# Kernel tuning notes

Hardware: AMD Instinct MI355X
Metric: run time of the kernel (lower is better)

The kernel has to match this reference:

```python
import jax, jax.numpy as jnp
import numpy as np

K = 20          # num neighbors (init kwarg k)
BN_EPS = 1e-5   # PyTorch BatchNorm default eps


def setup_inputs() -> dict:
    key = jax.random.key(0)
    k1, k2 = jax.random.split(key, 2)
    x = jax.random.normal(k1, (8, 64, 4096), dtype=jnp.float32)       # (b, d, n)
    w = jax.random.normal(k2, (64, 128), dtype=jnp.float32) * 0.05    # Conv2d 1x1: (out=64, in=2*64)
    gamma = jnp.ones((64,), jnp.float32)    # BatchNorm1d weight
    beta = jnp.zeros((64,), jnp.float32)    # BatchNorm1d bias
    return {"x": x, "w": w, "gamma": gamma, "beta": beta}


def reference(x, w, gamma, beta):
    # x: (b, d, n)
    xt = jnp.swapaxes(x, 1, 2)                       # (b, n, d)
    # kNN via pairwise squared euclidean distance (same ordering as torch.cdist)
    sq = jnp.sum(xt * xt, axis=-1)                   # (b, n)
    d2 = sq[:, :, None] + sq[:, None, :] - 2.0 * jnp.einsum('bnd,bmd->bnm', xt, xt)
    _, idx = jax.lax.top_k(-d2, K)                   # (b, n, K) smallest distances
    # gather neighbor features: (b, n, K, d)
    nb = jax.vmap(lambda pts, i: pts[i])(xt, idx)
    ctr = xt[:, :, None, :]                          # (b, n, 1, d)
    # edge feature = concat([neighbor - x, x]) -> (b, n, K, 2d)
    feat = jnp.concatenate([nb - ctr, jnp.broadcast_to(ctr, nb.shape)], axis=-1)
    # 1x1 conv (no bias) then max over neighbors
    h = jnp.max(jnp.einsum('bnkc,oc->bnko', feat, w), axis=2)   # (b, n, out)
    # BatchNorm1d (training mode: batch statistics over (b, n), biased var)
    mean = jnp.mean(h, axis=(0, 1))
    var = jnp.mean((h - mean) ** 2, axis=(0, 1))
    hn = (h - mean) / jnp.sqrt(var + BN_EPS) * gamma + beta
    out = jax.nn.gelu(hn, approximate=False)         # exact GELU (PyTorch default)
    return jnp.swapaxes(out, 1, 2)                   # (b, out, n)
```

## Files before the change

### kernel.cpp

```cpp
#include <hip/hip_runtime.h>

#define BIGF 3.402823466e38f

typedef __attribute__((ext_vector_type(8))) short bf16x8;
typedef __attribute__((ext_vector_type(4))) float f32x4;

__device__ __forceinline__ void gload_lds16(const float* g, float* lds) {
  __builtin_amdgcn_global_load_lds((const __attribute__((address_space(1))) void*)g,
                                   (__attribute__((address_space(3))) void*)lds, 16, 0, 0);
}
__device__ __forceinline__ void gload_lds16u(const unsigned short* g, unsigned short* lds) {
  __builtin_amdgcn_global_load_lds((const __attribute__((address_space(1))) void*)g,
                                   (__attribute__((address_space(3))) void*)lds, 16, 0, 0);
}

__device__ __forceinline__ unsigned short bf16_rne(float f) {
  unsigned int u = __float_as_uint(f);
  return (unsigned short)((u + 0x7fffu + ((u >> 16) & 1u)) >> 16);
}

__global__ __launch_bounds__(256) void k1_pre(const float* __restrict__ x, const float* __restrict__ w,
                                              float* __restrict__ sq, float* __restrict__ y,
                                              float* __restrict__ delta, unsigned short* __restrict__ xhl) {
  __shared__ __align__(16) float xt[64][68];
  __shared__ __align__(16) float ws[128][64];
  const int t = threadIdx.x;
  const int bid = blockIdx.x;
  const int b = bid >> 6;
  const int n0 = (bid & 63) << 6;
  const float* xb = x + (size_t)b * 64 * 4096;

#pragma unroll
  for (int rep = 0; rep < 16; ++rep) {
    int id = rep * 256 + t;
    int d = id >> 6, n = id & 63;
    xt[n][d] = xb[(size_t)d * 4096 + n0 + n];
  }
#pragma unroll
  for (int rep = 0; rep < 32; ++rep) {
    int id = rep * 256 + t;
    int u = id >> 6, dd = id & 63;
    ws[u][dd] = w[(u & 63) * 128 + ((u >> 6) << 6) + dd];
  }
  __syncthreads();

  {
    const int p = t >> 2;
    const int cg = t & 3;
    uint4* orow = (uint4*)xhl + ((size_t)(b << 12) + n0 + p) * 16;
#pragma unroll
    for (int cc = 0; cc < 4; ++cc) {
      const int c = cg * 4 + cc;
      const int kb = (c & 7) * 8;
      const bool lohalf = (c >= 8);
      unsigned int pk[4];
#pragma unroll
      for (int j2 = 0; j2 < 4; ++j2) {
        unsigned short u0, u1;
#pragma unroll
        for (int e = 0; e < 2; ++e) {
          const float xv = xt[p][kb + j2 * 2 + e];
          unsigned short h = bf16_rne(xv);
          unsigned short r;
          if (!lohalf) r = h;
          else r = bf16_rne(xv - __uint_as_float(((unsigned int)h) << 16));
          if (e == 0) u0 = r; else u1 = r;
        }
        pk[j2] = (unsigned int)u0 | ((unsigned int)u1 << 16);
      }
      uint4 v;
      v.x = pk[0]; v.y = pk[1]; v.z = pk[2]; v.w = pk[3];
      orow[c ^ (p & 7)] = v;
    }
  }

  const int p = t & 63;
  const int oc = t >> 6;
  float accy[16], accz[16];
#pragma unroll
  for (int j = 0; j < 16; ++j) { accy[j] = 0.f; accz[j] = 0.f; }

#pragma unroll 4
  for (int d4 = 0; d4 < 16; ++d4) {
    const float4 xv = *(const float4*)&xt[p][d4 * 4];
#pragma unroll
    for (int j = 0; j < 16; ++j) {
      const int o = oc * 16 + j;
      const float4 wy = *(const float4*)&ws[o][d4 * 4];
      const float4 wz = *(const float4*)&ws[o + 64][d4 * 4];
      accy[j] = fmaf(xv.x, wy.x, fmaf(xv.y, wy.y, fmaf(xv.z, wy.z, fmaf(xv.w, wy.w, accy[j]))));
      accz[j] = fmaf(xv.x, wz.x, fmaf(xv.y, wz.y, fmaf(xv.z, wz.z, fmaf(xv.w, wz.w, accz[j]))));
    }
  }

  if (oc == 0) {
    float s = 0.f;
#pragma unroll
    for (int d4 = 0; d4 < 16; ++d4) {
      const float4 v = *(const float4*)&xt[p][d4 * 4];
      s = fmaf(v.x, v.x, fmaf(v.y, v.y, fmaf(v.z, v.z, fmaf(v.w, v.w, s))));
    }
    sq[b * 4096 + n0 + p] = s;
  }

  const size_t row = ((size_t)b * 4096 + n0 + p) * 64 + oc * 16;
#pragma unroll
  for (int j4 = 0; j4 < 4; ++j4) {
    float4 yv = make_float4(accy[j4 * 4], accy[j4 * 4 + 1], accy[j4 * 4 + 2], accy[j4 * 4 + 3]);
    float4 dv = make_float4(accz[j4 * 4] - accy[j4 * 4], accz[j4 * 4 + 1] - accy[j4 * 4 + 1],
                            accz[j4 * 4 + 2] - accy[j4 * 4 + 2], accz[j4 * 4 + 3] - accy[j4 * 4 + 3]);
    *(float4*)&y[row + j4 * 4] = yv;
    *(float4*)&delta[row + j4 * 4] = dv;
  }
}

__global__ __launch_bounds__(256, 2) void k2_knn(const unsigned short* __restrict__ xhl,
                                                 const float* __restrict__ sq,
                                                 int* __restrict__ idx_out) {
  __shared__ __align__(16) float smem[4096 + 8192 + 6656];
  const int t = threadIdx.x;
  const int lane = t & 63;
  const int w = t >> 6;
  float* BsW = smem + 4096 + (w << 11);
  uint4* BsW4 = (uint4*)BsW;
  const uint4* As4 = (const uint4*)smem;
  uint2* bufL = (uint2*)(smem + 12288) + ((w << 6) + lane) * 13;

  const int bid = blockIdx.x;
  const int b = bid >> 6;
  const int n0 = (bid & 63) << 6;
  const int pn = lane & 15, q = lane >> 4;

  const unsigned short* xr = xhl + ((size_t)(b << 12)) * 128;
  const float* sqb = sq + (b << 12);

  {
    unsigned short* asu = (unsigned short*)smem;
#pragma unroll
    for (int qq = 0; qq < 4; ++qq) {
      const int kk = w * 4 + qq;
      gload_lds16u(xr + (size_t)n0 * 128 + kk * 512 + lane * 8, asu + kk * 512);
    }
  }
  __syncthreads();

  bf16x8 bfr[4][4];
#pragma unroll
  for (int nt = 0; nt < 4; ++nt)
#pragma unroll
    for (int j = 0; j < 4; ++j)
      bfr[nt][j] = *reinterpret_cast<const bf16x8*>(&As4[((nt << 4) + pn) * 16 + (((j << 2) + q) ^ (pn & 7))]);

  float kd[20];
  int ki[20];
#pragma unroll
  for (int s = 0; s < 20; ++s) { kd[s] = BIGF; ki[s] = -1; }
  const float sqn = sqb[n0 + lane];
  const int myn = lane;
  const int swz = myn & 7;
  int cnt = 0;

  auto ins = [&](float vd, int vi) {
#pragma unroll
    for (int s = 0; s < 20; ++s) {
      const float od = kd[s];
      const int oi = ki[s];
      const bool lt = vd < od;
      kd[s] = lt ? vd : od;
      ki[s] = lt ? vi : oi;
      vd = lt ? od : vd;
      vi = lt ? oi : vi;
    }
  };

  auto drain = [&]() {
#pragma unroll 1
    for (int j = 0; j < 12; ++j) {
      if (!__any(j < cnt)) break;
      if (j < cnt) {
        const uint2 e = bufL[j];
        const float dv = __uint_as_float(e.x);
        if (dv < kd[19]) ins(dv, (int)e.y);
      }
    }
    cnt = 0;
  };

  const f32x4 zero4 = {0.f, 0.f, 0.f, 0.f};
  f32x4 acc[4][2];
#pragma unroll
  for (int nt = 0; nt < 4; ++nt) { acc[nt][0] = zero4; acc[nt][1] = zero4; }

  for (int kt = 0; kt < 32; ++kt) {
    const int mbase = (w + 4 * kt) << 5;
    {
      unsigned short* bsu = (unsigned short*)BsW;
      const unsigned short* src = xr + (size_t)mbase * 128;
#pragma unroll
      for (int k = 0; k < 8; ++k) gload_lds16u(src + k * 512 + lane * 8, bsu + k * 512);
    }
    const f32x4 sqm0 = *(const f32x4*)&sqb[mbase + (q << 2)];
    const f32x4 sqm1 = *(const f32x4*)&sqb[mbase + 16 + (q << 2)];
    __builtin_amdgcn_s_waitcnt(0x0F70);

#pragma unroll
    for (int mt = 0; mt < 2; ++mt) {
      bf16x8 afr[4];
#pragma unroll
      for (int j = 0; j < 4; ++j)
        afr[j] = *reinterpret_cast<const bf16x8*>(&BsW4[((mt << 4) + pn) * 16 + (((j << 2) + q) ^ (pn & 7))]);
#pragma unroll
      for (int nt = 0; nt < 4; ++nt) {
        f32x4 a = acc[nt][mt];
        a = __builtin_amdgcn_mfma_f32_16x16x32_bf16(afr[0], bfr[nt][0], a, 0, 0, 0);
        a = __builtin_amdgcn_mfma_f32_16x16x32_bf16(afr[1], bfr[nt][1], a, 0, 0, 0);
        a = __builtin_amdgcn_mfma_f32_16x16x32_bf16(afr[0], bfr[nt][2], a, 0, 0, 0);
        a = __builtin_amdgcn_mfma_f32_16x16x32_bf16(afr[1], bfr[nt][3], a, 0, 0, 0);
        a = __builtin_amdgcn_mfma_f32_16x16x32_bf16(afr[2], bfr[nt][0], a, 0, 0, 0);
        a = __builtin_amdgcn_mfma_f32_16x16x32_bf16(afr[3], bfr[nt][1], a, 0, 0, 0);
        acc[nt][mt] = a;
      }
    }

#pragma unroll
    for (int nt = 0; nt < 4; ++nt) {
#pragma unroll
      for (int mt = 0; mt < 2; ++mt) {
        const int n = (nt << 4) + pn;
        const int g = (mt << 2) + q;
        const int pc = g ^ (n & 7);
        const f32x4 sv = mt ? sqm1 : sqm0;
        f32x4 dv = sv - 2.0f * acc[nt][mt];
        *(f32x4*)&BsW[(n << 5) + (pc << 2)] = dv;
        acc[nt][mt] = zero4;
      }
    }

#pragma unroll 1
    for (int cc = 0; cc < 8; ++cc) {
      const float4 v = *(const float4*)&BsW[(myn << 5) + ((cc ^ swz) << 2)];
      const int mb = mbase + (cc << 2);
      const float c0 = sqn + v.x, c1 = sqn + v.y, c2 = sqn + v.z, c3 = sqn + v.w;
      const float thr = kd[19];
      const float mn = fminf(fminf(c0, c1), fminf(c2, c3));
      if (mn < thr) {
        if (c0 < thr) { bufL[cnt] = make_uint2(__float_as_uint(c0), (unsigned)mb); cnt++; }
        if (c1 < thr) { bufL[cnt] = make_uint2(__float_as_uint(c1), (unsigned)(mb + 1)); cnt++; }
        if (c2 < thr) { bufL[cnt] = make_uint2(__float_as_uint(c2), (unsigned)(mb + 2)); cnt++; }
        if (c3 < thr) { bufL[cnt] = make_uint2(__float_as_uint(c3), (unsigned)(mb + 3)); cnt++; }
      }
      if (__any(cnt > 8)) drain();
    }
  }
  drain();

  __syncthreads();
  float* pf = smem;
  int* pi = (int*)(smem + 5120);
#pragma unroll
  for (int s = 0; s < 20; ++s) {
    pf[(w * 20 + s) * 64 + lane] = kd[s];
    pi[(w * 20 + s) * 64 + lane] = ki[s];
  }
  __syncthreads();
  if (w == 0) {
    auto insTie = [&](float vd, int vi) {
#pragma unroll
      for (int s = 0; s < 20; ++s) {
        const float od = kd[s];
        const int oi = ki[s];
        const bool lt = (vd < od) || (vd == od && vi < oi);
        kd[s] = lt ? vd : od;
        ki[s] = lt ? vi : oi;
        vd = lt ? od : vd;
        vi = lt ? oi : vi;
      }
    };
    for (int ww = 1; ww < 4; ++ww) {
#pragma unroll 1
      for (int s = 0; s < 20; ++s) {
        const float dv = pf[(ww * 20 + s) * 64 + lane];
        const int iv = pi[(ww * 20 + s) * 64 + lane];
        if (dv < kd[19] || (dv == kd[19] && iv < ki[19])) insTie(dv, iv);
      }
    }
    int* orow = idx_out + ((size_t)(b << 12) + n0 + lane) * 20;
#pragma unroll
    for (int s = 0; s < 20; ++s) orow[s] = ki[s];
  }
}

__global__ __launch_bounds__(256) void k3_gather(const float* __restrict__ y,
                                                 const float* __restrict__ delta,
                                                 const int* __restrict__ idx,
                                                 float* __restrict__ h,
                                                 float* __restrict__ sums,
                                                 float* __restrict__ sumsq) {
  const int t = threadIdx.x;
  const int lane = t & 63;
  const int w = t >> 6;
  const int blk = blockIdx.x;
  float s1 = 0.f, s2 = 0.f;
  for (int p = 0; p < 16; ++p) {
    const int ng = blk * 64 + w * 16 + p;
    const int b = ng >> 12;
    const int* row = idx + (size_t)ng * 20;
    float mx = -BIGF;
#pragma unroll
    for (int kk = 0; kk < 20; ++kk) {
      const int nbr = row[kk];
      mx = fmaxf(mx, y[((size_t)(b << 12) + nbr) * 64 + lane]);
    }
    const float hv = mx + delta[(size_t)ng * 64 + lane];
    h[(size_t)ng * 64 + lane] = hv;
    s1 += hv;
    s2 += hv * hv;
  }
  __shared__ float r1[4][64], r2[4][64];
  r1[w][lane] = s1;
  r2[w][lane] = s2;
  __syncthreads();
  if (w == 0) {
    const float a = r1[0][lane] + r1[1][lane] + r1[2][lane] + r1[3][lane];
    const float c = r2[0][lane] + r2[1][lane] + r2[2][lane] + r2[3][lane];
    atomicAdd(&sums[lane], a);
    atomicAdd(&sumsq[lane], c);
  }
}

__global__ __launch_bounds__(256) void k4_bn(const float* __restrict__ h,
                                             const float* __restrict__ sums,
                                             const float* __restrict__ sumsq,
                                             const float* __restrict__ gamma,
                                             const float* __restrict__ beta,
                                             float* __restrict__ out) {
  __shared__ float tile[64][65];
  const int bid = blockIdx.x;
  const int b = bid >> 6;
  const int n0 = (bid & 63) << 6;
  const int t = threadIdx.x;
  const int o = t & 63;
#pragma unroll
  for (int it = 0; it < 16; ++it) {
    const int n = (t >> 6) * 16 + it;
    tile[n][o] = h[(((size_t)b << 12) + n0 + n) * 64 + o];
  }
  __syncthreads();
  const int j = t & 63;
#pragma unroll
  for (int it = 0; it < 16; ++it) {
    const int oo = (t >> 6) * 16 + it;
    const float mean = sums[oo] * (1.0f / 32768.0f);
    const float var = sumsq[oo] * (1.0f / 32768.0f) - mean * mean;
    const float sc = gamma[oo] / sqrtf(var + 1e-5f);
    const float hv = tile[j][oo];
    const float hn = (hv - mean) * sc + beta[oo];
    const float g = 0.5f * hn * (1.0f + erff(hn * 0.70710678118654752f));
    out[((size_t)(b * 64 + oo)) * 4096 + n0 + j] = g;
  }
}

extern "C" void kernel_launch(void* const* d_in, const int* in_sizes, int n_in,
                              void* d_out, int out_size, void* d_ws, size_t ws_size,
                              hipStream_t stream) {
  const float* x = (const float*)d_in[0];
  const float* w = (const float*)d_in[1];
  const float* gamma = (const float*)d_in[2];
  const float* beta = (const float*)d_in[3];
  float* out = (float*)d_out;

  float* sq_ws = (float*)d_ws;
  float* y_ws = sq_ws + 32768;
  float* delta_ws = y_ws + 2097152;
  float* h_ws = delta_ws + 2097152;
  int* idx_ws = (int*)(h_ws + 2097152);
  float* sums = (float*)(idx_ws + 655360);
  float* sumsq = sums + 64;
  unsigned short* xhl = (unsigned short*)h_ws;

  hipMemsetAsync(sums, 0, 2 * 64 * sizeof(float), stream);
  k1_pre<<<512, 256, 0, stream>>>(x, w, sq_ws, y_ws, delta_ws, xhl);
  k2_knn<<<512, 256, 0, stream>>>(xhl, sq_ws, idx_ws);
  k3_gather<<<512, 256, 0, stream>>>(y_ws, delta_ws, idx_ws, h_ws, sums, sumsq);
  k4_bn<<<512, 256, 0, stream>>>(h_ws, sums, sumsq, gamma, beta, out);
}
```

Measured before the change: 346.9 us.

## Double-buffer kNN candidate tiles with smaller slices and vectorize gather loads

The kNN kernel now stages 16-column candidate tiles per wave into two alternating LDS buffers. The next tile's global-to-LDS load is issued before the MFMA and selection work on the current tile, hiding load latency behind compute. The A-tile LDS region is reused after the fragments are loaded into registers, which cuts shared memory footprint; the candidate buffer shrinks and is drained more often. Separately, the gather kernel reads neighbor rows as float4 with 16 threads per point instead of scalar loads, which reduces the number of memory instructions.

```diff
diff --git a/kernel.cpp b/kernel.cpp
--- a/kernel.cpp
+++ b/kernel.cpp
@@ -5,10 +5,6 @@
 typedef __attribute__((ext_vector_type(8))) short bf16x8;
 typedef __attribute__((ext_vector_type(4))) float f32x4;
 
-__device__ __forceinline__ void gload_lds16(const float* g, float* lds) {
-  __builtin_amdgcn_global_load_lds((const __attribute__((address_space(1))) void*)g,
-                                   (__attribute__((address_space(3))) void*)lds, 16, 0, 0);
-}
 __device__ __forceinline__ void gload_lds16u(const unsigned short* g, unsigned short* lds) {
   __builtin_amdgcn_global_load_lds((const __attribute__((address_space(1))) void*)g,
                                    (__attribute__((address_space(3))) void*)lds, 16, 0, 0);
@@ -117,15 +113,10 @@
 __global__ __launch_bounds__(256, 2) void k2_knn(const unsigned short* __restrict__ xhl,
                                                  const float* __restrict__ sq,
                                                  int* __restrict__ idx_out) {
-  __shared__ __align__(16) float smem[4096 + 8192 + 6656];
+  __shared__ __align__(16) float smem[12800];
   const int t = threadIdx.x;
   const int lane = t & 63;
   const int w = t >> 6;
-  float* BsW = smem + 4096 + (w << 11);
-  uint4* BsW4 = (uint4*)BsW;
-  const uint4* As4 = (const uint4*)smem;
-  uint2* bufL = (uint2*)(smem + 12288) + ((w << 6) + lane) * 13;
-
   const int bid = blockIdx.x;
   const int b = bid >> 6;
   const int n0 = (bid & 63) << 6;
@@ -145,11 +136,18 @@
   __syncthreads();
 
   bf16x8 bfr[4][4];
-#pragma unroll
-  for (int nt = 0; nt < 4; ++nt)
-#pragma unroll
-    for (int j = 0; j < 4; ++j)
-      bfr[nt][j] = *reinterpret_cast<const bf16x8*>(&As4[((nt << 4) + pn) * 16 + (((j << 2) + q) ^ (pn & 7))]);
+  {
+    const uint4* As4 = (const uint4*)smem;
+#pragma unroll
+    for (int nt = 0; nt < 4; ++nt)
+#pragma unroll
+      for (int j = 0; j < 4; ++j)
+        bfr[nt][j] = *reinterpret_cast<const bf16x8*>(&As4[((nt << 4) + pn) * 16 + (((j << 2) + q) ^ (pn & 7))]);
+  }
+  __syncthreads();
+
+  float* const sliceBase = smem + (w << 11);
+  uint2* bufL = (uint2*)(smem + 8192) + ((w << 6) + lane) * 9;
 
   float kd[20];
   int ki[20];
@@ -157,7 +155,7 @@
   for (int s = 0; s < 20; ++s) { kd[s] = BIGF; ki[s] = -1; }
   const float sqn = sqb[n0 + lane];
   const int myn = lane;
-  const int swz = myn & 7;
+  const int sw2 = (myn >> 1) & 3;
   int cnt = 0;
 
   auto ins = [&](float vd, int vi) {
@@ -175,7 +173,7 @@
 
   auto drain = [&]() {
 #pragma unroll 1
-    for (int j = 0; j < 12; ++j) {
+    for (int j = 0; j < 9; ++j) {
       if (!__any(j < cnt)) break;
       if (j < cnt) {
         const uint2 e = bufL[j];
@@ -186,59 +184,63 @@
     cnt = 0;
   };
 
+  auto stageM = [&](int mb, float* dst) {
+    unsigned short* du = (unsigned short*)dst;
+    const unsigned short* src = xr + (size_t)mb * 128;
+#pragma unroll
+    for (int k = 0; k < 4; ++k) gload_lds16u(src + k * 512 + lane * 8, du + k * 512);
+  };
+
   const f32x4 zero4 = {0.f, 0.f, 0.f, 0.f};
-  f32x4 acc[4][2];
-#pragma unroll
-  for (int nt = 0; nt < 4; ++nt) { acc[nt][0] = zero4; acc[nt][1] = zero4; }
-
-  for (int kt = 0; kt < 32; ++kt) {
-    const int mbase = (w + 4 * kt) << 5;
-    {
-      unsigned short* bsu = (unsigned short*)BsW;
-      const unsigned short* src = xr + (size_t)mbase * 128;
-#pragma unroll
-      for (int k = 0; k < 8; ++k) gload_lds16u(src + k * 512 + lane * 8, bsu + k * 512);
-    }
-    const f32x4 sqm0 = *(const f32x4*)&sqb[mbase + (q << 2)];
-    const f32x4 sqm1 = *(const f32x4*)&sqb[mbase + 16 + (q << 2)];
+
+  stageM((w) << 4, sliceBase);
+  f32x4 sqm_cur = *(const f32x4*)&sqb[((w) << 4) + (q << 2)];
+
+  int par = 0;
+  for (int kt = 0; kt < 64; ++kt) {
+    const int mbase = (w + 4 * kt) << 4;
+    float* Bs = sliceBase + (par << 10);
     __builtin_amdgcn_s_waitcnt(0x0F70);
 
-#pragma unroll
-    for (int mt = 0; mt < 2; ++mt) {
-      bf16x8 afr[4];
-#pragma unroll
-      for (int j = 0; j < 4; ++j)
-        afr[j] = *reinterpret_cast<const bf16x8*>(&BsW4[((mt << 4) + pn) * 16 + (((j << 2) + q) ^ (pn & 7))]);
-#pragma unroll
-      for (int nt = 0; nt < 4; ++nt) {
-        f32x4 a = acc[nt][mt];
-        a = __builtin_amdgcn_mfma_f32_16x16x32_bf16(afr[0], bfr[nt][0], a, 0, 0, 0);
-        a = __builtin_amdgcn_mfma_f32_16x16x32_bf16(afr[1], bfr[nt][1], a, 0, 0, 0);
-        a = __builtin_amdgcn_mfma_f32_16x16x32_bf16(afr[0], bfr[nt][2], a, 0, 0, 0);
-        a = __builtin_amdgcn_mfma_f32_16x16x32_bf16(afr[1], bfr[nt][3], a, 0, 0, 0);
-        a = __builtin_amdgcn_mfma_f32_16x16x32_bf16(afr[2], bfr[nt][0], a, 0, 0, 0);
-        a = __builtin_amdgcn_mfma_f32_16x16x32_bf16(afr[3], bfr[nt][1], a, 0, 0, 0);
-        acc[nt][mt] = a;
-      }
-    }
-
+    const uint4* Bs4 = (const uint4*)Bs;
+    bf16x8 afr[4];
+#pragma unroll
+    for (int j = 0; j < 4; ++j)
+      afr[j] = *reinterpret_cast<const bf16x8*>(&Bs4[pn * 16 + (((j << 2) + q) ^ (pn & 7))]);
+
+    f32x4 sqm_next;
+    if (kt + 1 < 64) {
+      const int mnext = (w + 4 * (kt + 1)) << 4;
+      stageM(mnext, sliceBase + ((par ^ 1) << 10));
+      sqm_next = *(const f32x4*)&sqb[mnext + (q << 2)];
+    }
+
+    f32x4 acc[4];
+#pragma unroll
+    for (int nt = 0; nt < 4; ++nt) acc[nt] = zero4;
 #pragma unroll
     for (int nt = 0; nt < 4; ++nt) {
-#pragma unroll
-      for (int mt = 0; mt < 2; ++mt) {
-        const int n = (nt << 4) + pn;
-        const int g = (mt << 2) + q;
-        const int pc = g ^ (n & 7);
-        const f32x4 sv = mt ? sqm1 : sqm0;
-        f32x4 dv = sv - 2.0f * acc[nt][mt];
-        *(f32x4*)&BsW[(n << 5) + (pc << 2)] = dv;
-        acc[nt][mt] = zero4;
-      }
+      f32x4 a = acc[nt];
+      a = __builtin_amdgcn_mfma_f32_16x16x32_bf16(afr[0], bfr[nt][0], a, 0, 0, 0);
+      a = __builtin_amdgcn_mfma_f32_16x16x32_bf16(afr[1], bfr[nt][1], a, 0, 0, 0);
+      a = __builtin_amdgcn_mfma_f32_16x16x32_bf16(afr[0], bfr[nt][2], a, 0, 0, 0);
+      a = __builtin_amdgcn_mfma_f32_16x16x32_bf16(afr[1], bfr[nt][3], a, 0, 0, 0);
+      a = __builtin_amdgcn_mfma_f32_16x16x32_bf16(afr[2], bfr[nt][0], a, 0, 0, 0);
+      a = __builtin_amdgcn_mfma_f32_16x16x32_bf16(afr[3], bfr[nt][1], a, 0, 0, 0);
+      acc[nt] = a;
+    }
+
+#pragma unroll
+    for (int nt = 0; nt < 4; ++nt) {
+      const int n = (nt << 4) + pn;
+      const int pc = q ^ ((n >> 1) & 3);
+      f32x4 dv = sqm_cur - 2.0f * acc[nt];
+      *(f32x4*)&Bs[(n << 4) + (pc << 2)] = dv;
     }
 
 #pragma unroll 1
-    for (int cc = 0; cc < 8; ++cc) {
-      const float4 v = *(const float4*)&BsW[(myn << 5) + ((cc ^ swz) << 2)];
+    for (int cc = 0; cc < 4; ++cc) {
+      const float4 v = *(const float4*)&Bs[(myn << 4) + ((cc ^ sw2) << 2)];
       const int mb = mbase + (cc << 2);
       const float c0 = sqn + v.x, c1 = sqn + v.y, c2 = sqn + v.z, c3 = sqn + v.w;
       const float thr = kd[19];
@@ -249,8 +251,10 @@
         if (c2 < thr) { bufL[cnt] = make_uint2(__float_as_uint(c2), (unsigned)(mb + 2)); cnt++; }
         if (c3 < thr) { bufL[cnt] = make_uint2(__float_as_uint(c3), (unsigned)(mb + 3)); cnt++; }
       }
-      if (__any(cnt > 8)) drain();
-    }
+      if (__any(cnt > 4)) drain();
+    }
+    sqm_cur = sqm_next;
+    par ^= 1;
   }
   drain();
 
@@ -296,35 +300,40 @@
                                                  float* __restrict__ h,
                                                  float* __restrict__ sums,
                                                  float* __restrict__ sumsq) {
+  __shared__ float r1[16][64], r2[16][64];
   const int t = threadIdx.x;
-  const int lane = t & 63;
-  const int w = t >> 6;
+  const int cg = t & 15;
+  const int pw = t >> 4;
   const int blk = blockIdx.x;
-  float s1 = 0.f, s2 = 0.f;
-  for (int p = 0; p < 16; ++p) {
-    const int ng = blk * 64 + w * 16 + p;
+  float4 s1 = make_float4(0.f, 0.f, 0.f, 0.f), s2 = s1;
+#pragma unroll 1
+  for (int pp = 0; pp < 4; ++pp) {
+    const int ng = blk * 64 + pw * 4 + pp;
     const int b = ng >> 12;
     const int* row = idx + (size_t)ng * 20;
-    float mx = -BIGF;
+    float4 mx = make_float4(-BIGF, -BIGF, -BIGF, -BIGF);
 #pragma unroll
     for (int kk = 0; kk < 20; ++kk) {
       const int nbr = row[kk];
-      mx = fmaxf(mx, y[((size_t)(b << 12) + nbr) * 64 + lane]);
-    }
-    const float hv = mx + delta[(size_t)ng * 64 + lane];
-    h[(size_t)ng * 64 + lane] = hv;
-    s1 += hv;
-    s2 += hv * hv;
-  }
-  __shared__ float r1[4][64], r2[4][64];
-  r1[w][lane] = s1;
-  r2[w][lane] = s2;
-  __syncthreads();
-  if (w == 0) {
-    const float a = r1[0][lane] + r1[1][lane] + r1[2][lane] + r1[3][lane];
-    const float c = r2[0][lane] + r2[1][lane] + r2[2][lane] + r2[3][lane];
-    atomicAdd(&sums[lane], a);
-    atomicAdd(&sumsq[lane], c);
+      const float4 v = *(const float4*)&y[(((size_t)(b << 12)) + nbr) * 64 + cg * 4];
+      mx.x = fmaxf(mx.x, v.x); mx.y = fmaxf(mx.y, v.y);
+      mx.z = fmaxf(mx.z, v.z); mx.w = fmaxf(mx.w, v.w);
+    }
+    const float4 dl = *(const float4*)&delta[(size_t)ng * 64 + cg * 4];
+    float4 hv = make_float4(mx.x + dl.x, mx.y + dl.y, mx.z + dl.z, mx.w + dl.w);
+    *(float4*)&h[(size_t)ng * 64 + cg * 4] = hv;
+    s1.x += hv.x; s1.y += hv.y; s1.z += hv.z; s1.w += hv.w;
+    s2.x += hv.x * hv.x; s2.y += hv.y * hv.y; s2.z += hv.z * hv.z; s2.w += hv.w * hv.w;
+  }
+  *(float4*)&r1[pw][cg * 4] = s1;
+  *(float4*)&r2[pw][cg * 4] = s2;
+  __syncthreads();
+  if (t < 64) {
+    float a = 0.f, c = 0.f;
+#pragma unroll
+    for (int i = 0; i < 16; ++i) { a += r1[i][t]; c += r2[i][t]; }
+    atomicAdd(&sums[t], a);
+    atomicAdd(&sumsq[t], c);
   }
 }
 
```

Result: slower. 373.3 us (+7.6%).
